# Kernel tuning notes

Measured on AMD Instinct MI355X. Metric: run time of the kernel, lower is better.

The kernel has to match this reference:

```python
import jax, jax.numpy as jnp
import numpy as np

B = 1; H = 256; W = 256; C = 192; HEADS = 6; WS = 16; SHIFT = 8
N = WS * WS; HD = C // HEADS; HID = 4 * C


def setup_inputs() -> dict:
    key = jax.random.key(0)
    ks = jax.random.split(key, 8)
    # relative position index (standard Swin construction)
    coords = np.stack(np.meshgrid(np.arange(WS), np.arange(WS), indexing='ij'))  # 2,ws,ws
    cf = coords.reshape(2, -1)
    rel = (cf[:, :, None] - cf[:, None, :]).transpose(1, 2, 0)  # n,n,2
    rel[..., 0] += WS - 1
    rel[..., 1] += WS - 1
    rel[..., 0] *= 2 * WS - 1
    rpi = rel.sum(-1).astype(np.int32)  # [N,N], values in [0, (2*WS-1)^2)
    # shifted-window attention mask (standard Swin construction)
    img = np.zeros((1, H, W, 1), np.float32)
    cnt = 0
    sl = (slice(0, -WS), slice(-WS, -SHIFT), slice(-SHIFT, None))
    for hs in sl:
        for ws_ in sl:
            img[:, hs, ws_, :] = cnt
            cnt += 1
    mw = img.reshape(1, H // WS, WS, W // WS, WS, 1).transpose(0, 1, 3, 2, 4, 5).reshape(-1, N)
    diff = mw[:, None, :] - mw[:, :, None]  # [nw, N, N]
    attn_mask = np.where(diff != 0, np.float32(-100.0), np.float32(0.0))
    std = 0.02
    p = lambda k, shp: jax.random.normal(k, shp, jnp.float32) * std
    return {
        'x': jax.random.normal(ks[0], (B, H * W, C), jnp.float32),
        'rpi_sa': jnp.asarray(rpi),
        'attn_mask': jnp.asarray(attn_mask),
        'norm1_g': jnp.ones((C,), jnp.float32), 'norm1_b': jnp.zeros((C,), jnp.float32),
        'qkv_w': p(ks[1], (C, 3 * C)), 'qkv_b': jnp.zeros((3 * C,), jnp.float32),
        'rpb_table': p(ks[2], ((2 * WS - 1) * (2 * WS - 1), HEADS)),
        'proj_w': p(ks[3], (C, C)), 'proj_b': jnp.zeros((C,), jnp.float32),
        'norm2_g': jnp.ones((C,), jnp.float32), 'norm2_b': jnp.zeros((C,), jnp.float32),
        'fc1_w': p(ks[4], (C, HID)), 'fc1_b': jnp.zeros((HID,), jnp.float32),
        'fc2_w': p(ks[5], (HID, C)), 'fc2_b': jnp.zeros((C,), jnp.float32),
    }


def _ln(x, g, b):
    m = x.mean(-1, keepdims=True)
    v = ((x - m) ** 2).mean(-1, keepdims=True)
    return (x - m) * jax.lax.rsqrt(v + 1e-5) * g + b


def reference(x, rpi_sa, attn_mask, norm1_g, norm1_b, qkv_w, qkv_b, rpb_table,
              proj_w, proj_b, norm2_g, norm2_b, fc1_w, fc1_b, fc2_w, fc2_b):
    b = x.shape[0]
    shortcut = x
    h = _ln(x, norm1_g, norm1_b).reshape(b, H, W, C)
    h = jnp.roll(h, (-SHIFT, -SHIFT), axis=(1, 2))
    # window partition -> (b*nw, N, C)
    xw = h.reshape(b, H // WS, WS, W // WS, WS, C).transpose(0, 1, 3, 2, 4, 5).reshape(-1, N, C)
    qkv = (xw @ qkv_w + qkv_b).reshape(-1, N, 3, HEADS, HD).transpose(2, 0, 3, 1, 4)
    q, k, v = qkv[0] * (HD ** -0.5), qkv[1], qkv[2]  # [b_, H, N, HD]
    attn = jnp.einsum('bhnd,bhmd->bhnm', q, k)  # [b_, H, N, N]
    bias = rpb_table[rpi_sa.reshape(-1)].reshape(N, N, HEADS).transpose(2, 0, 1)
    attn = attn + bias[None]
    nw = attn_mask.shape[0]
    attn = attn.reshape(-1, nw, HEADS, N, N) + attn_mask[None, :, None]
    attn = jax.nn.softmax(attn.reshape(-1, HEADS, N, N), axis=-1)
    out = jnp.einsum('bhnm,bhmd->bnhd', attn, v).reshape(-1, N, C)
    out = out @ proj_w + proj_b
    # window reverse + unshift
    out = out.reshape(b, H // WS, W // WS, WS, WS, C).transpose(0, 1, 3, 2, 4, 5).reshape(b, H, W, C)
    out = jnp.roll(out, (SHIFT, SHIFT), axis=(1, 2)).reshape(b, H * W, C)
    xr = shortcut + out  # drop_path = identity (eval / drop_prob=0)
    y = _ln(xr, norm2_g, norm2_b)
    y = jax.nn.gelu(y @ fc1_w + fc1_b, approximate=False) @ fc2_w + fc2_b
    return xr + y
```

## Files before the change

### kernel.cpp

```cpp
#include <hip/hip_runtime.h>
#include <math.h>

#define NHEADS 6
#define CC 192
#define HDIM 32
#define NTOK 256
#define SHIFTV 8

typedef __attribute__((ext_vector_type(8))) short short8;
typedef __attribute__((ext_vector_type(4))) short short4v;
typedef __attribute__((ext_vector_type(4))) float floatx4;

__device__ inline short f2bf(float f) {
    union { float f; unsigned u; } v; v.f = f;
    unsigned r = (v.u + 0x7FFFu + ((v.u >> 16) & 1u)) >> 16;
    return (short)r;
}

__device__ inline float gelu_f(float x) {
    float x2 = x * x;
    float p = x * (-1.5957691216f - 0.07135481627f * x2);
    float e = __expf(p);
    return x * __builtin_amdgcn_rcpf(1.f + e);
}

__global__ __launch_bounds__(256) void bias_kernel(const int* __restrict__ rpi,
                                                   const float* __restrict__ rpb,
                                                   float* __restrict__ biasB) {
    int idx = blockIdx.x * 256 + threadIdx.x;
    int m = idx & 255;
    int n = (idx >> 8) & 255;
    int h = idx >> 16;
    biasB[idx] = rpb[rpi[n * 256 + m] * NHEADS + h];
}

__global__ __launch_bounds__(256) void cvt_kernel(const float* __restrict__ qkvw,
                                                  const float* __restrict__ pw,
                                                  const float* __restrict__ f1w,
                                                  const float* __restrict__ f2w,
                                                  short* __restrict__ wqt,
                                                  short* __restrict__ pwt,
                                                  short* __restrict__ w1t,
                                                  short* __restrict__ w2t) {
    int idx = blockIdx.x * 256 + threadIdx.x;
    int n = idx / 192, k = idx - n * 192;
    w1t[idx] = f2bf(f1w[k * 768 + n]);
    int c = idx / 768, h = idx - c * 768;
    w2t[idx] = f2bf(f2w[h * 192 + c]);
    if (idx < 576 * 192) wqt[idx] = f2bf(qkvw[k * 576 + n]);
    if (idx < 192 * 192) pwt[idx] = f2bf(pw[k * 192 + n]);
}

__global__ __launch_bounds__(256) void qkv_kernel(const float* __restrict__ x,
        const float* __restrict__ g1, const float* __restrict__ b1,
        const short* __restrict__ wqt, const float* __restrict__ qkvb,
        ushort* __restrict__ Qb, ushort* __restrict__ Kb, ushort* __restrict__ VTb) {
    __shared__ __align__(16) short xln[64 * 200];
    __shared__ float red[64][4][2];
    const int t = threadIdx.x;
    const int g0 = blockIdx.x * 64;
    const int w = g0 >> 8;
    {
        int row = t >> 2, part = t & 3;
        int n = (g0 + row) & 255;
        int sy = (((w >> 4) << 4) + (n >> 4) + SHIFTV) & 255;
        int sx = (((w & 15) << 4) + (n & 15) + SHIFTV) & 255;
        const float* xr = x + (sy * 256 + sx) * CC + part * 48;
        float vals[48];
        float s = 0.f, ss = 0.f;
        #pragma unroll
        for (int i = 0; i < 48; ++i) { float v = xr[i]; vals[i] = v; s += v; ss += v * v; }
        red[row][part][0] = s; red[row][part][1] = ss;
        __syncthreads();
        float sum = red[row][0][0] + red[row][1][0] + red[row][2][0] + red[row][3][0];
        float sq  = red[row][0][1] + red[row][1][1] + red[row][2][1] + red[row][3][1];
        float mean = sum * (1.f / 192.f);
        float var = sq * (1.f / 192.f) - mean * mean;
        float inv = rsqrtf(var + 1e-5f);
        #pragma unroll
        for (int i = 0; i < 48; ++i) {
            int c = part * 48 + i;
            xln[row * 200 + c] = f2bf((vals[i] - mean) * inv * g1[c] + b1[c]);
        }
    }
    __syncthreads();
    const int wv = t >> 6, lane = t & 63;
    const int lr = lane & 15;
    const int lk = (lane >> 4) * 8;
    const int q4 = (lane >> 4) * 4;
    #pragma unroll
    for (int jc = 0; jc < 3; ++jc) {
        floatx4 acc[4][3];
        #pragma unroll
        for (int mt = 0; mt < 4; ++mt)
            #pragma unroll
            for (int nt = 0; nt < 3; ++nt) acc[mt][nt] = floatx4{0.f,0.f,0.f,0.f};
        for (int ks = 0; ks < 6; ++ks) {
            int k0 = ks * 32 + lk;
            short8 a[4];
            #pragma unroll
            for (int mt = 0; mt < 4; ++mt)
                a[mt] = *(const short8*)&xln[(mt * 16 + lr) * 200 + k0];
            #pragma unroll
            for (int nt = 0; nt < 3; ++nt) {
                int nglob = jc * 192 + wv * 48 + nt * 16 + lr;
                short8 b = *(const short8*)&wqt[nglob * 192 + k0];
                #pragma unroll
                for (int mt = 0; mt < 4; ++mt)
                    acc[mt][nt] = __builtin_amdgcn_mfma_f32_16x16x32_bf16(a[mt], b, acc[mt][nt], 0, 0, 0);
            }
        }
        #pragma unroll
        for (int nt = 0; nt < 3; ++nt) {
            int jj = wv * 48 + nt * 16 + lr;
            float bias = qkvb[jc * 192 + jj];
            int head = jj >> 5, hd = jj & 31;
            int wh = w * NHEADS + head;
            #pragma unroll
            for (int mt = 0; mt < 4; ++mt) {
                int nr0 = (g0 + mt * 16 + q4) & 255;
                if (jc == 0) {
                    #pragma unroll
                    for (int reg = 0; reg < 4; ++reg)
                        Qb[((size_t)wh * NTOK + nr0 + reg) * HDIM + hd] =
                            (ushort)f2bf((acc[mt][nt][reg] + bias) * 0.17677669529663687f);
                } else if (jc == 1) {
                    #pragma unroll
                    for (int reg = 0; reg < 4; ++reg)
                        Kb[((size_t)wh * NTOK + nr0 + reg) * HDIM + hd] =
                            (ushort)f2bf(acc[mt][nt][reg] + bias);
                } else {
                    short4v pk;
                    #pragma unroll
                    for (int reg = 0; reg < 4; ++reg)
                        pk[reg] = f2bf(acc[mt][nt][reg] + bias);
                    *(short4v*)&VTb[((size_t)wh * HDIM + hd) * NTOK + nr0] = pk;
                }
            }
        }
    }
}

__global__ __launch_bounds__(256) void attn_kernel(const ushort* __restrict__ Q,
        const ushort* __restrict__ K, const ushort* __restrict__ VT,
        const float* __restrict__ biasB, const float* __restrict__ mask,
        ushort* __restrict__ Ob) {
    __shared__ __align__(16) ushort Ks[256 * 40];
    __shared__ __align__(16) ushort Vs[32 * 264];
    __shared__ __align__(16) ushort Ps[4][64 * 40];
    const int t = threadIdx.x;
    const int wh = blockIdx.x;
    const int w = wh / 6, h = wh - w * 6;
    {
        const ushort* kg = K + (size_t)wh * (NTOK * HDIM);
        const ushort* vg = VT + (size_t)wh * (NTOK * HDIM);
        for (int i = t * 8; i < NTOK * HDIM; i += 2048) {
            short8 kv = *(const short8*)(kg + i);
            *(short8*)&Ks[(i >> 5) * 40 + (i & 31)] = kv;
            short8 vv = *(const short8*)(vg + i);
            *(short8*)&Vs[(i >> 8) * 264 + (i & 255)] = vv;
        }
    }
    const int wv = t >> 6, lane = t & 63;
    const int lc = lane & 15;
    const int q4 = (lane >> 4) * 4;
    const int lk8 = (lane >> 4) * 8;
    const int qb = wv * 64;
    short8 qf[4];
    {
        const ushort* qg = Q + (size_t)wh * (NTOK * HDIM);
        #pragma unroll
        for (int qt = 0; qt < 4; ++qt)
            qf[qt] = *(const short8*)(qg + (qb + qt * 16 + lc) * HDIM + lk8);
    }
    __syncthreads();
    float Ssum[4];
    floatx4 o[2][4];
    #pragma unroll
    for (int qt = 0; qt < 4; ++qt) {
        Ssum[qt] = 0.f;
        o[0][qt] = floatx4{0.f,0.f,0.f,0.f};
        o[1][qt] = floatx4{0.f,0.f,0.f,0.f};
    }
    ushort* Pw = &Ps[wv][0];
    const float* bp = biasB + h * 65536;
    const float* mp = mask + (size_t)w * 65536;
    for (int kc = 0; kc < 8; ++kc) {
        const int k0 = kc * 32;
        short8 ka[2];
        ka[0] = *(const short8*)&Ks[(k0 + lc) * 40 + lk8];
        ka[1] = *(const short8*)&Ks[(k0 + 16 + lc) * 40 + lk8];
        floatx4 sf[2][4];
        #pragma unroll
        for (int kt = 0; kt < 2; ++kt)
            #pragma unroll
            for (int qt = 0; qt < 4; ++qt)
                sf[kt][qt] = __builtin_amdgcn_mfma_f32_16x16x32_bf16(ka[kt], qf[qt],
                                floatx4{0.f,0.f,0.f,0.f}, 0, 0, 0);
        #pragma unroll
        for (int kt = 0; kt < 2; ++kt)
            #pragma unroll
            for (int qt = 0; qt < 4; ++qt) {
                int q = qb + qt * 16 + lc;
                int kbase = k0 + kt * 16 + q4;
                float4 bb = *(const float4*)(bp + q * 256 + kbase);
                float4 mm = *(const float4*)(mp + q * 256 + kbase);
                float p0 = __expf(sf[kt][qt][0] + bb.x + mm.x);
                float p1 = __expf(sf[kt][qt][1] + bb.y + mm.y);
                float p2 = __expf(sf[kt][qt][2] + bb.z + mm.z);
                float p3 = __expf(sf[kt][qt][3] + bb.w + mm.w);
                Ssum[qt] += (p0 + p1) + (p2 + p3);
                short4v pk;
                pk.x = f2bf(p0); pk.y = f2bf(p1); pk.z = f2bf(p2); pk.w = f2bf(p3);
                *(short4v*)&Pw[(qt * 16 + lc) * 40 + kt * 16 + q4] = pk;
            }
        short8 va[2], pf[4];
        va[0] = *(const short8*)&Vs[lc * 264 + k0 + lk8];
        va[1] = *(const short8*)&Vs[(16 + lc) * 264 + k0 + lk8];
        #pragma unroll
        for (int qt = 0; qt < 4; ++qt)
            pf[qt] = *(const short8*)&Pw[(qt * 16 + lc) * 40 + lk8];
        #pragma unroll
        for (int ht = 0; ht < 2; ++ht)
            #pragma unroll
            for (int qt = 0; qt < 4; ++qt)
                o[ht][qt] = __builtin_amdgcn_mfma_f32_16x16x32_bf16(va[ht], pf[qt], o[ht][qt], 0, 0, 0);
    }
    #pragma unroll
    for (int qt = 0; qt < 4; ++qt) {
        float rs = Ssum[qt];
        rs += __shfl_xor(rs, 16);
        rs += __shfl_xor(rs, 32);
        float inv = 1.f / rs;
        size_t rowbase = ((size_t)(w * NTOK + qb + qt * 16 + lc)) * CC + h * HDIM;
        #pragma unroll
        for (int ht = 0; ht < 2; ++ht)
            #pragma unroll
            for (int r = 0; r < 4; ++r)
                Ob[rowbase + ht * 16 + q4 + r] = (ushort)f2bf(o[ht][qt][r] * inv);
    }
}

__global__ __launch_bounds__(256) void proj_kernel(const ushort* __restrict__ Ob,
        const short* __restrict__ pwt, const float* __restrict__ pb,
        const float* __restrict__ x, float* __restrict__ out) {
    __shared__ __align__(16) short oln[64 * 200];
    const int t = threadIdx.x;
    const int g0 = blockIdx.x * 64;
    const int w = g0 >> 8;
    {
        int row = t >> 2, part = t & 3;
        const ushort* orow = Ob + (size_t)(g0 + row) * CC + part * 48;
        #pragma unroll
        for (int i = 0; i < 6; ++i)
            *(short8*)&oln[row * 200 + part * 48 + i * 8] = *(const short8*)(orow + i * 8);
    }
    __syncthreads();
    const int wv = t >> 6, lane = t & 63;
    const int lr = lane & 15;
    const int lk = (lane >> 4) * 8;
    const int q4 = (lane >> 4) * 4;
    floatx4 acc[4][3];
    #pragma unroll
    for (int mt = 0; mt < 4; ++mt)
        #pragma unroll
        for (int nt = 0; nt < 3; ++nt) acc[mt][nt] = floatx4{0.f,0.f,0.f,0.f};
    for (int ks = 0; ks < 6; ++ks) {
        int k0 = ks * 32 + lk;
        short8 a[4];
        #pragma unroll
        for (int mt = 0; mt < 4; ++mt)
            a[mt] = *(const short8*)&oln[(mt * 16 + lr) * 200 + k0];
        #pragma unroll
        for (int nt = 0; nt < 3; ++nt) {
            int c = wv * 48 + nt * 16 + lr;
            short8 b = *(const short8*)&pwt[c * 192 + k0];
            #pragma unroll
            for (int mt = 0; mt < 4; ++mt)
                acc[mt][nt] = __builtin_amdgcn_mfma_f32_16x16x32_bf16(a[mt], b, acc[mt][nt], 0, 0, 0);
        }
    }
    #pragma unroll
    for (int nt = 0; nt < 3; ++nt) {
        int c = wv * 48 + nt * 16 + lr;
        float bias = pb[c];
        #pragma unroll
        for (int mt = 0; mt < 4; ++mt) {
            #pragma unroll
            for (int reg = 0; reg < 4; ++reg) {
                int nn = (g0 + mt * 16 + q4 + reg) & 255;
                int sy = (((w >> 4) << 4) + (nn >> 4) + SHIFTV) & 255;
                int sx = (((w & 15) << 4) + (nn & 15) + SHIFTV) & 255;
                size_t base = (size_t)(sy * 256 + sx) * CC;
                out[base + c] = x[base + c] + acc[mt][nt][reg] + bias;
            }
        }
    }
}

__global__ __launch_bounds__(256) void mlp_kernel(const float* __restrict__ g2,
        const float* __restrict__ b2, const short* __restrict__ w1t,
        const float* __restrict__ f1b, const short* __restrict__ w2t,
        const float* __restrict__ f2b, float* __restrict__ out) {
    __shared__ __align__(16) short xln[64 * 200];
    __shared__ __align__(16) short Hs[64 * 200];
    __shared__ float red[64][4][2];
    const int t = threadIdx.x;
    const int m0 = blockIdx.x * 64;
    {
        int row = t >> 2, part = t & 3;
        const float* xr = out + (size_t)(m0 + row) * CC + part * 48;
        float vals[48];
        float s = 0.f, ss = 0.f;
        #pragma unroll
        for (int i = 0; i < 48; ++i) { float v = xr[i]; vals[i] = v; s += v; ss += v * v; }
        red[row][part][0] = s; red[row][part][1] = ss;
        __syncthreads();
        float sum = red[row][0][0] + red[row][1][0] + red[row][2][0] + red[row][3][0];
        float sq  = red[row][0][1] + red[row][1][1] + red[row][2][1] + red[row][3][1];
        float mean = sum * (1.f / 192.f);
        float var = sq * (1.f / 192.f) - mean * mean;
        float inv = rsqrtf(var + 1e-5f);
        #pragma unroll
        for (int i = 0; i < 48; ++i) {
            int c = part * 48 + i;
            xln[row * 200 + c] = f2bf((vals[i] - mean) * inv * g2[c] + b2[c]);
        }
    }
    __syncthreads();
    const int wv = t >> 6;
    const int lane = t & 63;
    const int lr = lane & 15;
    const int lk = (lane >> 4) * 8;
    const int q4 = (lane >> 4) * 4;
    floatx4 acc2[4][3];
    #pragma unroll
    for (int mt = 0; mt < 4; ++mt)
        #pragma unroll
        for (int nt = 0; nt < 3; ++nt) acc2[mt][nt] = floatx4{0.f, 0.f, 0.f, 0.f};

    for (int hc = 0; hc < 4; ++hc) {
        floatx4 acc1[4][3];
        #pragma unroll
        for (int mt = 0; mt < 4; ++mt)
            #pragma unroll
            for (int nt = 0; nt < 3; ++nt) acc1[mt][nt] = floatx4{0.f, 0.f, 0.f, 0.f};
        for (int ks = 0; ks < 6; ++ks) {
            int k0 = ks * 32 + lk;
            short8 a[4];
            #pragma unroll
            for (int mt = 0; mt < 4; ++mt)
                a[mt] = *(const short8*)&xln[(mt * 16 + lr) * 200 + k0];
            #pragma unroll
            for (int nt = 0; nt < 3; ++nt) {
                int n = hc * 192 + wv * 48 + nt * 16 + lr;
                short8 b = *(const short8*)&w1t[n * 192 + k0];
                #pragma unroll
                for (int mt = 0; mt < 4; ++mt)
                    acc1[mt][nt] = __builtin_amdgcn_mfma_f32_16x16x32_bf16(a[mt], b, acc1[mt][nt], 0, 0, 0);
            }
        }
        __syncthreads();
        #pragma unroll
        for (int nt = 0; nt < 3; ++nt) {
            int colb = wv * 48 + nt * 16 + lr;
            float bias = f1b[hc * 192 + colb];
            #pragma unroll
            for (int mt = 0; mt < 4; ++mt) {
                #pragma unroll
                for (int reg = 0; reg < 4; ++reg) {
                    float v = acc1[mt][nt][reg] + bias;
                    Hs[(mt * 16 + q4 + reg) * 200 + colb] = f2bf(gelu_f(v));
                }
            }
        }
        __syncthreads();
        for (int ks = 0; ks < 6; ++ks) {
            int k0 = ks * 32 + lk;
            short8 a[4];
            #pragma unroll
            for (int mt = 0; mt < 4; ++mt)
                a[mt] = *(const short8*)&Hs[(mt * 16 + lr) * 200 + k0];
            #pragma unroll
            for (int nt = 0; nt < 3; ++nt) {
                int c = wv * 48 + nt * 16 + lr;
                short8 b = *(const short8*)&w2t[c * 768 + hc * 192 + k0];
                #pragma unroll
                for (int mt = 0; mt < 4; ++mt)
                    acc2[mt][nt] = __builtin_amdgcn_mfma_f32_16x16x32_bf16(a[mt], b, acc2[mt][nt], 0, 0, 0);
            }
        }
    }
    #pragma unroll
    for (int nt = 0; nt < 3; ++nt) {
        int c = wv * 48 + nt * 16 + lr;
        float bias = f2b[c];
        #pragma unroll
        for (int mt = 0; mt < 4; ++mt) {
            #pragma unroll
            for (int reg = 0; reg < 4; ++reg) {
                size_t off = (size_t)(m0 + mt * 16 + q4 + reg) * CC + c;
                out[off] = out[off] + acc2[mt][nt][reg] + bias;
            }
        }
    }
}

extern "C" void kernel_launch(void* const* d_in, const int* in_sizes, int n_in,
                              void* d_out, int out_size, void* d_ws, size_t ws_size,
                              hipStream_t stream) {
    (void)in_sizes; (void)n_in; (void)out_size; (void)ws_size;
    const float* x    = (const float*)d_in[0];
    const int*   rpi  = (const int*)d_in[1];
    const float* mask = (const float*)d_in[2];
    const float* n1g  = (const float*)d_in[3];
    const float* n1b  = (const float*)d_in[4];
    const float* qkvw = (const float*)d_in[5];
    const float* qkvb = (const float*)d_in[6];
    const float* rpb  = (const float*)d_in[7];
    const float* pw   = (const float*)d_in[8];
    const float* pb   = (const float*)d_in[9];
    const float* n2g  = (const float*)d_in[10];
    const float* n2b  = (const float*)d_in[11];
    const float* f1w  = (const float*)d_in[12];
    const float* f1b  = (const float*)d_in[13];
    const float* f2w  = (const float*)d_in[14];
    const float* f2b  = (const float*)d_in[15];
    float* out = (float*)d_out;

    ushort* Qb  = (ushort*)d_ws;
    ushort* Kb  = Qb + 12582912;
    ushort* VTb = Kb + 12582912;
    ushort* Ob  = VTb + 12582912;
    float* BIAS = (float*)(Ob + 12582912);
    short* WQT  = (short*)(BIAS + 393216);
    short* PWT  = WQT + 110592;
    short* W1T  = PWT + 36864;
    short* W2T  = W1T + 147456;

    bias_kernel<<<1536, 256, 0, stream>>>(rpi, rpb, BIAS);
    cvt_kernel<<<576, 256, 0, stream>>>(qkvw, pw, f1w, f2w, WQT, PWT, W1T, W2T);
    qkv_kernel<<<1024, 256, 0, stream>>>(x, n1g, n1b, WQT, qkvb, Qb, Kb, VTb);
    attn_kernel<<<1536, 256, 0, stream>>>(Qb, Kb, VTb, BIAS, mask, Ob);
    proj_kernel<<<1024, 256, 0, stream>>>(Ob, PWT, pb, x, out);
    mlp_kernel<<<1024, 256, 0, stream>>>(n2g, n2b, W1T, f1b, W2T, f2b, out);
}
```

Measured before the change: 487.4 us.

## Restructure MLP kernel so each wave owns 16 tokens with per-wave hidden staging

The MLP kernel now gives each wave its own 16 tokens and walks the hidden dimension in chunks of 32. GELU results are staged in a small per-wave LDS buffer, which removes the block-wide __syncthreads and the large shared hidden buffer. The GEMMs are transposed so the weights become the MFMA A operand, which allows float4 bias loads and vectorized float4 residual stores. In exchange, every wave now re-reads all of W1 and W2 from global/L2 with less reuse across waves, and there are more small sequential MFMA chains.

After: 749.0 us. +53.7%, slower.

```diff
diff --git a/kernel.cpp b/kernel.cpp
--- a/kernel.cpp
+++ b/kernel.cpp
@@ -303,8 +303,8 @@
         const float* __restrict__ f1b, const short* __restrict__ w2t,
         const float* __restrict__ f2b, float* __restrict__ out) {
     __shared__ __align__(16) short xln[64 * 200];
-    __shared__ __align__(16) short Hs[64 * 200];
     __shared__ float red[64][4][2];
+    __shared__ __align__(16) ushort Hsw[4][16 * 40];
     const int t = threadIdx.x;
     const int m0 = blockIdx.x * 64;
     {
@@ -328,81 +328,59 @@
         }
     }
     __syncthreads();
-    const int wv = t >> 6;
-    const int lane = t & 63;
-    const int lr = lane & 15;
-    const int lk = (lane >> 4) * 8;
+    const int wv = t >> 6, lane = t & 63;
+    const int lc = lane & 15;
+    const int lk8 = (lane >> 4) * 8;
     const int q4 = (lane >> 4) * 4;
-    floatx4 acc2[4][3];
-    #pragma unroll
-    for (int mt = 0; mt < 4; ++mt)
-        #pragma unroll
-        for (int nt = 0; nt < 3; ++nt) acc2[mt][nt] = floatx4{0.f, 0.f, 0.f, 0.f};
-
-    for (int hc = 0; hc < 4; ++hc) {
-        floatx4 acc1[4][3];
-        #pragma unroll
-        for (int mt = 0; mt < 4; ++mt)
-            #pragma unroll
-            for (int nt = 0; nt < 3; ++nt) acc1[mt][nt] = floatx4{0.f, 0.f, 0.f, 0.f};
-        for (int ks = 0; ks < 6; ++ks) {
-            int k0 = ks * 32 + lk;
-            short8 a[4];
-            #pragma unroll
-            for (int mt = 0; mt < 4; ++mt)
-                a[mt] = *(const short8*)&xln[(mt * 16 + lr) * 200 + k0];
-            #pragma unroll
-            for (int nt = 0; nt < 3; ++nt) {
-                int n = hc * 192 + wv * 48 + nt * 16 + lr;
-                short8 b = *(const short8*)&w1t[n * 192 + k0];
-                #pragma unroll
-                for (int mt = 0; mt < 4; ++mt)
-                    acc1[mt][nt] = __builtin_amdgcn_mfma_f32_16x16x32_bf16(a[mt], b, acc1[mt][nt], 0, 0, 0);
-            }
-        }
-        __syncthreads();
-        #pragma unroll
-        for (int nt = 0; nt < 3; ++nt) {
-            int colb = wv * 48 + nt * 16 + lr;
-            float bias = f1b[hc * 192 + colb];
-            #pragma unroll
-            for (int mt = 0; mt < 4; ++mt) {
-                #pragma unroll
-                for (int reg = 0; reg < 4; ++reg) {
-                    float v = acc1[mt][nt][reg] + bias;
-                    Hs[(mt * 16 + q4 + reg) * 200 + colb] = f2bf(gelu_f(v));
-                }
-            }
-        }
-        __syncthreads();
-        for (int ks = 0; ks < 6; ++ks) {
-            int k0 = ks * 32 + lk;
-            short8 a[4];
-            #pragma unroll
-            for (int mt = 0; mt < 4; ++mt)
-                a[mt] = *(const short8*)&Hs[(mt * 16 + lr) * 200 + k0];
-            #pragma unroll
-            for (int nt = 0; nt < 3; ++nt) {
-                int c = wv * 48 + nt * 16 + lr;
-                short8 b = *(const short8*)&w2t[c * 768 + hc * 192 + k0];
-                #pragma unroll
-                for (int mt = 0; mt < 4; ++mt)
-                    acc2[mt][nt] = __builtin_amdgcn_mfma_f32_16x16x32_bf16(a[mt], b, acc2[mt][nt], 0, 0, 0);
-            }
-        }
-    }
-    #pragma unroll
-    for (int nt = 0; nt < 3; ++nt) {
-        int c = wv * 48 + nt * 16 + lr;
-        float bias = f2b[c];
-        #pragma unroll
-        for (int mt = 0; mt < 4; ++mt) {
-            #pragma unroll
-            for (int reg = 0; reg < 4; ++reg) {
-                size_t off = (size_t)(m0 + mt * 16 + q4 + reg) * CC + c;
-                out[off] = out[off] + acc2[mt][nt][reg] + bias;
-            }
-        }
+    short8 bx[6];
+    #pragma unroll
+    for (int ks = 0; ks < 6; ++ks)
+        bx[ks] = *(const short8*)&xln[(wv * 16 + lc) * 200 + ks * 32 + lk8];
+    ushort* Hw = &Hsw[wv][0];
+    floatx4 acc2[12];
+    #pragma unroll
+    for (int mt = 0; mt < 12; ++mt) acc2[mt] = floatx4{0.f,0.f,0.f,0.f};
+    for (int hc = 0; hc < 24; ++hc) {
+        const int h0 = hc * 32;
+        floatx4 a1[2];
+        #pragma unroll
+        for (int ht = 0; ht < 2; ++ht) {
+            const short* wr = &w1t[(h0 + ht * 16 + lc) * 192 + lk8];
+            floatx4 acc = floatx4{0.f,0.f,0.f,0.f};
+            #pragma unroll
+            for (int ks = 0; ks < 6; ++ks)
+                acc = __builtin_amdgcn_mfma_f32_16x16x32_bf16(
+                        *(const short8*)(wr + ks * 32), bx[ks], acc, 0, 0, 0);
+            a1[ht] = acc;
+        }
+        #pragma unroll
+        for (int ht = 0; ht < 2; ++ht) {
+            float4 bb = *(const float4*)&f1b[h0 + ht * 16 + q4];
+            short4v pk;
+            pk.x = f2bf(gelu_f(a1[ht][0] + bb.x));
+            pk.y = f2bf(gelu_f(a1[ht][1] + bb.y));
+            pk.z = f2bf(gelu_f(a1[ht][2] + bb.z));
+            pk.w = f2bf(gelu_f(a1[ht][3] + bb.w));
+            *(short4v*)&Hw[lc * 40 + ht * 16 + q4] = pk;
+        }
+        short8 bh = *(const short8*)&Hw[lc * 40 + lk8];
+        #pragma unroll
+        for (int mt = 0; mt < 12; ++mt) {
+            short8 a = *(const short8*)&w2t[(mt * 16 + lc) * 768 + h0 + lk8];
+            acc2[mt] = __builtin_amdgcn_mfma_f32_16x16x32_bf16(a, bh, acc2[mt], 0, 0, 0);
+        }
+    }
+    const size_t tok = (size_t)(m0 + wv * 16 + lc);
+    #pragma unroll
+    for (int mt = 0; mt < 12; ++mt) {
+        float4 bb = *(const float4*)&f2b[mt * 16 + q4];
+        float* op = &out[tok * CC + mt * 16 + q4];
+        float4 o = *(const float4*)op;
+        o.x += acc2[mt][0] + bb.x;
+        o.y += acc2[mt][1] + bb.y;
+        o.z += acc2[mt][2] + bb.z;
+        o.w += acc2[mt][3] + bb.w;
+        *(float4*)op = o;
     }
 }
 
```
